# Kernel tuning notes

Measured on AMD Instinct MI355X. Metric: run time of the kernel, lower is better.

Reference implementation:

```python
import jax, jax.numpy as jnp
import numpy as np

NUM_SLOTS = 4096
NUM_CLUSTER = 10
SLOT_DIM = 64
EPS = 1e-8
N_ITER = 3
LN_EPS = 1e-5


def _ln(x, g, b):
    m = jnp.mean(x, axis=-1, keepdims=True)
    v = jnp.var(x, axis=-1, keepdims=True)
    return (x - m) / jnp.sqrt(v + LN_EPS) * g + b


def setup_inputs() -> dict:
    key = jax.random.key(0)
    ks = jax.random.split(key, 24)
    d, S = SLOT_DIM, NUM_SLOTS
    s = d ** -0.5
    f32 = jnp.float32
    return {
        "cluster_centers": jax.random.normal(ks[0], (NUM_CLUSTER, d), f32),
        "Wk": jax.random.normal(ks[1], (d, d), f32) * s,
        "bk": jnp.zeros((d,), f32),
        "Wq": jax.random.normal(ks[2], (d, d), f32) * s,
        "bq": jnp.zeros((d,), f32),
        "Wv": jax.random.normal(ks[3], (d, d), f32) * s,
        "bv": jnp.zeros((d,), f32),
        "cc_g": jnp.ones((d,), f32),
        "cc_b": jnp.zeros((d,), f32),
        "W_ih": jax.random.normal(ks[4], (3 * d, d), f32) * s,
        "W_hh": jax.random.normal(ks[5], (3 * d, d), f32) * s,
        "b_ih": jnp.zeros((3 * d,), f32),
        "b_hh": jnp.zeros((3 * d,), f32),
        "ln_g": jnp.ones((d,), f32),
        "ln_b": jnp.zeros((d,), f32),
        "W1": jax.random.normal(ks[6], (2 * d, d), f32) * s,
        "b1": jnp.zeros((2 * d,), f32),
        "W2": jax.random.normal(ks[7], (d, 2 * d), f32) * (2 * d) ** -0.5,
        "b2": jnp.zeros((d,), f32),
        "Wa": jax.random.normal(ks[8], (S, d, d), f32) * s,
        "ba": jnp.zeros((S, d), f32),
        "Wb": jax.random.normal(ks[9], (S, d, d), f32) * s,
        "bb": jnp.zeros((S, d), f32),
    }


def reference(cluster_centers, Wk, bk, Wq, bq, Wv, bv, cc_g, cc_b,
              W_ih, W_hh, b_ih, b_hh, ln_g, ln_b, W1, b1, W2, b2,
              Wa, ba, Wb, bb):
    temp = SLOT_DIM ** -0.5
    k = cluster_centers @ Wk.T + bk          # [N, d]
    v = cluster_centers @ Wv.T + bv          # [N, d]
    cc = cluster_centers
    for _ in range(N_ITER):
        cc_prev = cc
        q = _ln(cc, cc_g, cc_b) @ Wq.T + bq  # [N, d]
        attn = jnp.einsum('nd,md->nm', k, q) * temp
        attn = jax.nn.softmax(attn, axis=0) + EPS
        attn = attn / jnp.sum(attn, axis=-1, keepdims=True)
        updates = attn @ v                   # [N, d]
        # PyTorch GRUCell
        gi = updates @ W_ih.T + b_ih
        gh = cc_prev @ W_hh.T + b_hh
        ir, iz, inn = jnp.split(gi, 3, axis=-1)
        hr, hz, hn = jnp.split(gh, 3, axis=-1)
        r = jax.nn.sigmoid(ir + hr)
        z = jax.nn.sigmoid(iz + hz)
        n = jnp.tanh(inn + r * hn)
        cc = (1.0 - z) * n + z * cc_prev
        # residual MLP
        h = _ln(cc, ln_g, ln_b)
        cc = cc + jax.nn.relu(h @ W1.T + b1) @ W2.T + b2
    # per-slot 2-layer MLP + max over the 10 clusters, vectorized over slots
    h = jax.nn.relu(jnp.einsum('sij,nj->sni', Wa, cc) + ba[:, None, :])  # [S, N, d]
    out = jnp.einsum('sij,snj->sni', Wb, h) + bb[:, None, :]             # [S, N, d]
    return jnp.max(out, axis=1)                                          # [S, d]
```

## Files before the change

kernel.cpp:

```cpp
#include <hip/hip_runtime.h>
#include <math.h>

#define NCLU 10
#define D    64
#define NSLOT 4096

typedef unsigned int   u32;
typedef unsigned short u16;

typedef __attribute__((ext_vector_type(8))) short  bf16x8;
typedef __attribute__((ext_vector_type(4))) float  f32x4;

__device__ __forceinline__ u16 f2bf_rne(float f) {
    u32 u = __float_as_uint(f);
    return (u16)((u + 0x7fffu + ((u >> 16) & 1u)) >> 16);
}

__device__ __forceinline__ float dotb64(const float* __restrict__ xrow, const float4* w4) {
    const float4* x4 = (const float4*)xrow;
    float a0 = 0.f, a1 = 0.f, a2 = 0.f, a3 = 0.f;
#pragma unroll
    for (int jj = 0; jj < 16; ++jj) {
        float4 xv = x4[jj], wv = w4[jj];
        a0 += wv.x * xv.x; a1 += wv.y * xv.y; a2 += wv.z * xv.z; a3 += wv.w * xv.w;
    }
    return (a0 + a1) + (a2 + a3);
}
__device__ __forceinline__ float dotb128(const float* __restrict__ xrow, const float4* w4) {
    const float4* x4 = (const float4*)xrow;
    float a0 = 0.f, a1 = 0.f, a2 = 0.f, a3 = 0.f;
#pragma unroll
    for (int jj = 0; jj < 32; ++jj) {
        float4 xv = x4[jj], wv = w4[jj];
        a0 += wv.x * xv.x; a1 += wv.y * xv.y; a2 += wv.z * xv.z; a3 += wv.w * xv.w;
    }
    return (a0 + a1) + (a2 + a3);
}

__device__ __forceinline__ float wred(float v) {
#pragma unroll
    for (int off = 32; off > 0; off >>= 1) v += __shfl_xor(v, off);
    return v;
}

__global__ __launch_bounds__(640) void phase1_kernel(
    const float* __restrict__ cc0,
    const float* __restrict__ Wk, const float* __restrict__ bk,
    const float* __restrict__ Wq, const float* __restrict__ bq,
    const float* __restrict__ Wv, const float* __restrict__ bv,
    const float* __restrict__ cc_g, const float* __restrict__ cc_b,
    const float* __restrict__ W_ih, const float* __restrict__ W_hh,
    const float* __restrict__ b_ih, const float* __restrict__ b_hh,
    const float* __restrict__ ln_g, const float* __restrict__ ln_b,
    const float* __restrict__ W1, const float* __restrict__ b1,
    const float* __restrict__ W2, const float* __restrict__ b2,
    float* __restrict__ cc_out)
{
    const int t = threadIdx.x;
    const int w = t >> 6;
    const int i = t & 63;

    __shared__ float ccl[NCLU][64];
    __shared__ float xl[NCLU][64];
    __shared__ float kl[NCLU][64];
    __shared__ float vl[NCLU][64];
    __shared__ float ql[NCLU][68];
    __shared__ float al[NCLU][12];
    __shared__ float ul[NCLU][64];
    __shared__ float hl[NCLU][64];
    __shared__ float tl[NCLU][128];
    __shared__ float gl[6][NCLU][64];
    __shared__ float dl[NCLU][64];

    const float g_cc = cc_g[i], b_cc = cc_b[i];
    const float g_ln = ln_g[i], b_ln = ln_b[i];

    const float* srcp;
    float bias0 = 0.f, biask = 0.f;
    if (w == 0)      { srcp = Wq + i * 64;                     bias0 = bq[i]; }
    else if (w <= 3) { srcp = W_ih + ((w - 1) * 64 + i) * 64;  bias0 = b_ih[(w - 1) * 64 + i]; }
    else if (w <= 6) { srcp = W_hh + ((w - 4) * 64 + i) * 64;  bias0 = b_hh[(w - 4) * 64 + i]; }
    else if (w == 7) { srcp = Wk + i * 64;                     biask = bk[i]; }
    else if (w == 8) { srcp = Wv + i * 64;                     biask = bv[i]; }
    else             { srcp = W2 + i * 128;                    bias0 = b2[i]; }

    float4 w4[32];
#pragma unroll
    for (int jj = 0; jj < 16; ++jj) w4[jj] = ((const float4*)srcp)[jj];
#pragma unroll
    for (int jj = 16; jj < 32; ++jj) w4[jj] = make_float4(0.f, 0.f, 0.f, 0.f);
    if (w == 9) {
#pragma unroll
        for (int jj = 16; jj < 32; ++jj) w4[jj] = ((const float4*)srcp)[jj];
    }

    float c = cc0[w * 64 + i];
    ccl[w][i] = c;
    __syncthreads();

    if (w == 7) {
#pragma unroll
        for (int n = 0; n < NCLU; ++n) kl[n][i] = dotb64(&ccl[n][0], w4) + biask;
    } else if (w == 8) {
#pragma unroll
        for (int n = 0; n < NCLU; ++n) vl[n][i] = dotb64(&ccl[n][0], w4) + biask;
    }
    __syncthreads();

    if (w == 7) {
        const float4* p = (const float4*)(W1 + i * 64);
#pragma unroll
        for (int jj = 0; jj < 16; ++jj) w4[jj] = p[jj];
        bias0 = b1[i];
    } else if (w == 8) {
        const float4* p = (const float4*)(W1 + (64 + i) * 64);
#pragma unroll
        for (int jj = 0; jj < 16; ++jj) w4[jj] = p[jj];
        bias0 = b1[64 + i];
    }

    for (int it = 0; it < 3; ++it) {
        {
            float s1 = wred(c), s2 = wred(c * c);
            float mu = s1 * (1.f / 64.f);
            float va = s2 * (1.f / 64.f) - mu * mu;
            xl[w][i] = (c - mu) * rsqrtf(va + 1e-5f) * g_cc + b_cc;
        }
        __syncthreads();

        if (w == 0) {
#pragma unroll
            for (int n = 0; n < NCLU; ++n) ql[n][i] = dotb64(&xl[n][0], w4) + bias0;
        } else if (w >= 4 && w <= 6) {
#pragma unroll
            for (int n = 0; n < NCLU; ++n) gl[w - 1][n][i] = dotb64(&ccl[n][0], w4) + bias0;
        }
        __syncthreads();

        if (i < NCLU) {
            const float4* kf = (const float4*)&kl[w][0];
            const float4* qf = (const float4*)&ql[i][0];
            float a0 = 0.f, a1 = 0.f, a2 = 0.f, a3 = 0.f;
#pragma unroll
            for (int jj = 0; jj < 16; ++jj) {
                float4 kv = kf[jj], qv = qf[jj];
                a0 += kv.x * qv.x; a1 += kv.y * qv.y; a2 += kv.z * qv.z; a3 += kv.w * qv.w;
            }
            al[w][i] = ((a0 + a1) + (a2 + a3)) * 0.125f;
        }
        __syncthreads();

        if (t < NCLU) {
            float mx = -1e30f;
#pragma unroll
            for (int nn = 0; nn < NCLU; ++nn) mx = fmaxf(mx, al[nn][t]);
            float e[NCLU]; float s = 0.f;
#pragma unroll
            for (int nn = 0; nn < NCLU; ++nn) { e[nn] = __expf(al[nn][t] - mx); s += e[nn]; }
            float inv = 1.f / s;
#pragma unroll
            for (int nn = 0; nn < NCLU; ++nn) al[nn][t] = e[nn] * inv + 1e-8f;
        }
        __syncthreads();
        if (t < NCLU) {
            float s = 0.f;
#pragma unroll
            for (int m = 0; m < NCLU; ++m) s += al[t][m];
            float inv = 1.f / s;
#pragma unroll
            for (int m = 0; m < NCLU; ++m) al[t][m] *= inv;
        }
        __syncthreads();

        {
            float u = 0.f;
#pragma unroll
            for (int m = 0; m < NCLU; ++m) u += al[w][m] * vl[m][i];
            ul[w][i] = u;
        }
        __syncthreads();

        if (w >= 1 && w <= 3) {
#pragma unroll
            for (int n = 0; n < NCLU; ++n) gl[w - 1][n][i] = dotb64(&ul[n][0], w4) + bias0;
        }
        __syncthreads();

        {
            float ir = gl[0][w][i], iz = gl[1][w][i], inn = gl[2][w][i];
            float hr = gl[3][w][i], hz = gl[4][w][i], hn = gl[5][w][i];
            float r = 1.f / (1.f + __expf(-(ir + hr)));
            float z = 1.f / (1.f + __expf(-(iz + hz)));
            float nn2 = tanhf(inn + r * hn);
            c = (1.f - z) * nn2 + z * c;
        }

        {
            float s1 = wred(c), s2 = wred(c * c);
            float mu = s1 * (1.f / 64.f);
            float va = s2 * (1.f / 64.f) - mu * mu;
            hl[w][i] = (c - mu) * rsqrtf(va + 1e-5f) * g_ln + b_ln;
        }
        __syncthreads();

        if (w == 7) {
#pragma unroll
            for (int n = 0; n < NCLU; ++n) tl[n][i] = fmaxf(dotb64(&hl[n][0], w4) + bias0, 0.f);
        } else if (w == 8) {
#pragma unroll
            for (int n = 0; n < NCLU; ++n) tl[n][64 + i] = fmaxf(dotb64(&hl[n][0], w4) + bias0, 0.f);
        }
        __syncthreads();

        if (w == 9) {
#pragma unroll
            for (int n = 0; n < NCLU; ++n) dl[n][i] = dotb128(&tl[n][0], w4) + bias0;
        }
        __syncthreads();

        c += dl[w][i];
        ccl[w][i] = c;
        __syncthreads();
    }

    cc_out[w * 64 + i] = c;
}

#define WSTRIDE 72
__global__ __launch_bounds__(64) void phase2_kernel(
    const float* __restrict__ Wa, const float* __restrict__ ba,
    const float* __restrict__ Wb, const float* __restrict__ bb,
    const float* __restrict__ cc, float* __restrict__ out)
{
    const int s = blockIdx.x;
    const int l = threadIdx.x;
    const int quad = l >> 4;
    const int lc   = l & 15;

    __shared__ u16 Wlds[64 * WSTRIDE];
    __shared__ u16 hT[16 * WSTRIDE];

    const float* wa = Wa + (size_t)s * 4096;
    const float* wb = Wb + (size_t)s * 4096;

    float4 rg[16];
#pragma unroll
    for (int cch = 0; cch < 16; ++cch)
        rg[cch] = *(const float4*)(wa + cch * 256 + l * 4);

#pragma unroll
    for (int cch = 0; cch < 16; ++cch) {
        int row = cch * 4 + quad;
        u32 p0 = (u32)f2bf_rne(rg[cch].x) | ((u32)f2bf_rne(rg[cch].y) << 16);
        u32 p1 = (u32)f2bf_rne(rg[cch].z) | ((u32)f2bf_rne(rg[cch].w) << 16);
        uint2 pk; pk.x = p0; pk.y = p1;
        *(uint2*)(&Wlds[row * WSTRIDE + lc * 4]) = pk;
    }

#pragma unroll
    for (int cch = 0; cch < 16; ++cch)
        rg[cch] = *(const float4*)(wb + cch * 256 + l * 4);

    f32x4 acc[4];
#pragma unroll
    for (int mt = 0; mt < 4; ++mt) acc[mt] = (f32x4){0.f, 0.f, 0.f, 0.f};

#pragma unroll
    for (int kt = 0; kt < 2; ++kt) {
        bf16x8 bf;
        if (lc < NCLU) {
            const float* cp = cc + lc * 64 + kt * 32 + quad * 8;
            float4 c0 = *(const float4*)cp;
            float4 c1 = *(const float4*)(cp + 4);
            bf[0] = (short)f2bf_rne(c0.x); bf[1] = (short)f2bf_rne(c0.y);
            bf[2] = (short)f2bf_rne(c0.z); bf[3] = (short)f2bf_rne(c0.w);
            bf[4] = (short)f2bf_rne(c1.x); bf[5] = (short)f2bf_rne(c1.y);
            bf[6] = (short)f2bf_rne(c1.z); bf[7] = (short)f2bf_rne(c1.w);
        } else {
#pragma unroll
            for (int j = 0; j < 8; ++j) bf[j] = 0;
        }
#pragma unroll
        for (int mt = 0; mt < 4; ++mt) {
            bf16x8 af = *(const bf16x8*)(&Wlds[(16 * mt + lc) * WSTRIDE + kt * 32 + quad * 8]);
            acc[mt] = __builtin_amdgcn_mfma_f32_16x16x32_bf16(af, bf, acc[mt], 0, 0, 0);
        }
    }

#pragma unroll
    for (int mt = 0; mt < 4; ++mt) {
        float4 bav = *(const float4*)(ba + s * 64 + 16 * mt + quad * 4);
        u16 h0 = f2bf_rne(fmaxf(acc[mt][0] + bav.x, 0.f));
        u16 h1 = f2bf_rne(fmaxf(acc[mt][1] + bav.y, 0.f));
        u16 h2 = f2bf_rne(fmaxf(acc[mt][2] + bav.z, 0.f));
        u16 h3 = f2bf_rne(fmaxf(acc[mt][3] + bav.w, 0.f));
        uint2 pk; pk.x = (u32)h0 | ((u32)h1 << 16); pk.y = (u32)h2 | ((u32)h3 << 16);
        *(uint2*)(&hT[lc * WSTRIDE + 16 * mt + quad * 4]) = pk;
    }

#pragma unroll
    for (int cch = 0; cch < 16; ++cch) {
        int row = cch * 4 + quad;
        u32 p0 = (u32)f2bf_rne(rg[cch].x) | ((u32)f2bf_rne(rg[cch].y) << 16);
        u32 p1 = (u32)f2bf_rne(rg[cch].z) | ((u32)f2bf_rne(rg[cch].w) << 16);
        uint2 pk; pk.x = p0; pk.y = p1;
        *(uint2*)(&Wlds[row * WSTRIDE + lc * 4]) = pk;
    }

    f32x4 acc2[4];
#pragma unroll
    for (int mt = 0; mt < 4; ++mt) acc2[mt] = (f32x4){0.f, 0.f, 0.f, 0.f};
#pragma unroll
    for (int kt = 0; kt < 2; ++kt) {
        bf16x8 bf = *(const bf16x8*)(&hT[lc * WSTRIDE + kt * 32 + quad * 8]);
#pragma unroll
        for (int mt = 0; mt < 4; ++mt) {
            bf16x8 af = *(const bf16x8*)(&Wlds[(16 * mt + lc) * WSTRIDE + kt * 32 + quad * 8]);
            acc2[mt] = __builtin_amdgcn_mfma_f32_16x16x32_bf16(af, bf, acc2[mt], 0, 0, 0);
        }
    }

    const float NEG = -3.0e38f;
#pragma unroll
    for (int mt = 0; mt < 4; ++mt) {
#pragma unroll
        for (int r = 0; r < 4; ++r) {
            float v = (lc < NCLU) ? acc2[mt][r] : NEG;
#pragma unroll
            for (int off = 1; off < 16; off <<= 1)
                v = fmaxf(v, __shfl_xor(v, off));
            acc2[mt][r] = v;
        }
    }

    if (lc < 4) {
#pragma unroll
        for (int mt = 0; mt < 4; ++mt) {
            int row = 16 * mt + 4 * quad + lc;
            out[s * 64 + row] = acc2[mt][lc] + bb[s * 64 + row];
        }
    }
}

extern "C" void kernel_launch(void* const* d_in, const int* in_sizes, int n_in,
                              void* d_out, int out_size, void* d_ws, size_t ws_size,
                              hipStream_t stream) {
    const float* cc0  = (const float*)d_in[0];
    const float* Wk   = (const float*)d_in[1];
    const float* bk   = (const float*)d_in[2];
    const float* Wq   = (const float*)d_in[3];
    const float* bq   = (const float*)d_in[4];
    const float* Wv   = (const float*)d_in[5];
    const float* bv   = (const float*)d_in[6];
    const float* ccg  = (const float*)d_in[7];
    const float* ccb  = (const float*)d_in[8];
    const float* Wih  = (const float*)d_in[9];
    const float* Whh  = (const float*)d_in[10];
    const float* bih  = (const float*)d_in[11];
    const float* bhh  = (const float*)d_in[12];
    const float* lng  = (const float*)d_in[13];
    const float* lnb  = (const float*)d_in[14];
    const float* W1   = (const float*)d_in[15];
    const float* b1   = (const float*)d_in[16];
    const float* W2   = (const float*)d_in[17];
    const float* b2   = (const float*)d_in[18];
    const float* Wa   = (const float*)d_in[19];
    const float* ba   = (const float*)d_in[20];
    const float* Wb   = (const float*)d_in[21];
    const float* bb   = (const float*)d_in[22];

    float* cc_ws = (float*)d_ws;
    float* out   = (float*)d_out;

    hipLaunchKernelGGL(phase1_kernel, dim3(1), dim3(640), 0, stream,
                       cc0, Wk, bk, Wq, bq, Wv, bv, ccg, ccb,
                       Wih, Whh, bih, bhh, lng, lnb, W1, b1, W2, b2, cc_ws);

    hipLaunchKernelGGL(phase2_kernel, dim3(NSLOT), dim3(64), 0, stream,
                       Wa, ba, Wb, bb, cc_ws, out);
}
```

Measured before the change: 261.3 us.

## Use bf16 MFMA for phase1 small matmuls and split W2 across two waves

Replaces the per-thread fp32 dot products in the cluster-update kernel with bf16 MFMA 16x16x32 matmuls. Weight fragments are packed to bf16 in registers, and LDS rows are padded to a stride of 68. The 128-wide W2 reduction is split between waves 8 and 9, with the two partial outputs summed. This shortens the serial dependency chain and cuts register pressure (launch bounds now request 3 blocks), at the cost of bf16 precision on the iterative GRU/MLP updates.

```diff
diff --git a/kernel.cpp b/kernel.cpp
--- a/kernel.cpp
+++ b/kernel.cpp
@@ -16,25 +16,13 @@
     return (u16)((u + 0x7fffu + ((u >> 16) & 1u)) >> 16);
 }
 
-__device__ __forceinline__ float dotb64(const float* __restrict__ xrow, const float4* w4) {
-    const float4* x4 = (const float4*)xrow;
-    float a0 = 0.f, a1 = 0.f, a2 = 0.f, a3 = 0.f;
-#pragma unroll
-    for (int jj = 0; jj < 16; ++jj) {
-        float4 xv = x4[jj], wv = w4[jj];
-        a0 += wv.x * xv.x; a1 += wv.y * xv.y; a2 += wv.z * xv.z; a3 += wv.w * xv.w;
-    }
-    return (a0 + a1) + (a2 + a3);
-}
-__device__ __forceinline__ float dotb128(const float* __restrict__ xrow, const float4* w4) {
-    const float4* x4 = (const float4*)xrow;
-    float a0 = 0.f, a1 = 0.f, a2 = 0.f, a3 = 0.f;
-#pragma unroll
-    for (int jj = 0; jj < 32; ++jj) {
-        float4 xv = x4[jj], wv = w4[jj];
-        a0 += wv.x * xv.x; a1 += wv.y * xv.y; a2 += wv.z * xv.z; a3 += wv.w * xv.w;
-    }
-    return (a0 + a1) + (a2 + a3);
+__device__ __forceinline__ bf16x8 pack8(float4 a, float4 b) {
+    bf16x8 r;
+    r[0] = (short)f2bf_rne(a.x); r[1] = (short)f2bf_rne(a.y);
+    r[2] = (short)f2bf_rne(a.z); r[3] = (short)f2bf_rne(a.w);
+    r[4] = (short)f2bf_rne(b.x); r[5] = (short)f2bf_rne(b.y);
+    r[6] = (short)f2bf_rne(b.z); r[7] = (short)f2bf_rne(b.w);
+    return r;
 }
 
 __device__ __forceinline__ float wred(float v) {
@@ -43,7 +31,74 @@
     return v;
 }
 
-__global__ __launch_bounds__(640) void phase1_kernel(
+__device__ __forceinline__ void load_afrags64(bf16x8 a[4][2], const float* __restrict__ W,
+                                              int lc, int quad) {
+#pragma unroll
+    for (int mt = 0; mt < 4; ++mt)
+#pragma unroll
+        for (int kt = 0; kt < 2; ++kt) {
+            const float* p = W + (16 * mt + lc) * 64 + kt * 32 + quad * 8;
+            a[mt][kt] = pack8(*(const float4*)p, *(const float4*)(p + 4));
+        }
+}
+
+__device__ __forceinline__ void load_afrags128(bf16x8 a[4][2], const float* __restrict__ W,
+                                               int ktbase, int lc, int quad) {
+#pragma unroll
+    for (int mt = 0; mt < 4; ++mt)
+#pragma unroll
+        for (int kt = 0; kt < 2; ++kt) {
+            const float* p = W + (16 * mt + lc) * 128 + (ktbase + kt) * 32 + quad * 8;
+            a[mt][kt] = pack8(*(const float4*)p, *(const float4*)(p + 4));
+        }
+}
+
+__device__ __forceinline__ bf16x8 bfrag(const float* __restrict__ xbase, int xstride,
+                                        int lc, int quad, int ktglob) {
+    if (lc < NCLU) {
+        const float* p = xbase + lc * xstride + ktglob * 32 + quad * 8;
+        return pack8(*(const float4*)p, *(const float4*)(p + 4));
+    }
+    bf16x8 z;
+#pragma unroll
+    for (int j = 0; j < 8; ++j) z[j] = 0;
+    return z;
+}
+
+__device__ __forceinline__ void mm_apply(const bf16x8 a[4][2], const float* __restrict__ xbase,
+                                         int xstride, int ktbase,
+                                         float* __restrict__ obase, int ostride, int ooff,
+                                         const float* __restrict__ bias, bool do_relu,
+                                         int lc, int quad) {
+    f32x4 acc[4];
+#pragma unroll
+    for (int mt = 0; mt < 4; ++mt) acc[mt] = (f32x4){0.f, 0.f, 0.f, 0.f};
+#pragma unroll
+    for (int kt = 0; kt < 2; ++kt) {
+        bf16x8 b = bfrag(xbase, xstride, lc, quad, ktbase + kt);
+#pragma unroll
+        for (int mt = 0; mt < 4; ++mt)
+            acc[mt] = __builtin_amdgcn_mfma_f32_16x16x32_bf16(a[mt][kt], b, acc[mt], 0, 0, 0);
+    }
+    if (lc < NCLU) {
+#pragma unroll
+        for (int mt = 0; mt < 4; ++mt) {
+            float4 o;
+            o.x = acc[mt][0]; o.y = acc[mt][1]; o.z = acc[mt][2]; o.w = acc[mt][3];
+            if (bias) {
+                float4 bv = *(const float4*)(bias + 16 * mt + 4 * quad);
+                o.x += bv.x; o.y += bv.y; o.z += bv.z; o.w += bv.w;
+            }
+            if (do_relu) {
+                o.x = fmaxf(o.x, 0.f); o.y = fmaxf(o.y, 0.f);
+                o.z = fmaxf(o.z, 0.f); o.w = fmaxf(o.w, 0.f);
+            }
+            *(float4*)(obase + lc * ostride + ooff + 16 * mt + 4 * quad) = o;
+        }
+    }
+}
+
+__global__ __launch_bounds__(640, 3) void phase1_kernel(
     const float* __restrict__ cc0,
     const float* __restrict__ Wk, const float* __restrict__ bk,
     const float* __restrict__ Wq, const float* __restrict__ bq,
@@ -59,65 +114,53 @@
     const int t = threadIdx.x;
     const int w = t >> 6;
     const int i = t & 63;
-
-    __shared__ float ccl[NCLU][64];
-    __shared__ float xl[NCLU][64];
-    __shared__ float kl[NCLU][64];
-    __shared__ float vl[NCLU][64];
+    const int quad = i >> 4;
+    const int lc   = i & 15;
+
+    __shared__ float ccl[NCLU][68];
+    __shared__ float xl[NCLU][68];
+    __shared__ float kl[NCLU][68];
+    __shared__ float vl[NCLU][68];
     __shared__ float ql[NCLU][68];
+    __shared__ float ul[NCLU][68];
+    __shared__ float hl[NCLU][68];
+    __shared__ float dl9[NCLU][68];
+    __shared__ float dl8[NCLU][68];
+    __shared__ float tl[NCLU][132];
+    __shared__ float gl[6][NCLU][68];
     __shared__ float al[NCLU][12];
-    __shared__ float ul[NCLU][64];
-    __shared__ float hl[NCLU][64];
-    __shared__ float tl[NCLU][128];
-    __shared__ float gl[6][NCLU][64];
-    __shared__ float dl[NCLU][64];
 
     const float g_cc = cc_g[i], b_cc = cc_b[i];
     const float g_ln = ln_g[i], b_ln = ln_b[i];
 
-    const float* srcp;
-    float bias0 = 0.f, biask = 0.f;
-    if (w == 0)      { srcp = Wq + i * 64;                     bias0 = bq[i]; }
-    else if (w <= 3) { srcp = W_ih + ((w - 1) * 64 + i) * 64;  bias0 = b_ih[(w - 1) * 64 + i]; }
-    else if (w <= 6) { srcp = W_hh + ((w - 4) * 64 + i) * 64;  bias0 = b_hh[(w - 4) * 64 + i]; }
-    else if (w == 7) { srcp = Wk + i * 64;                     biask = bk[i]; }
-    else if (w == 8) { srcp = Wv + i * 64;                     biask = bv[i]; }
-    else             { srcp = W2 + i * 128;                    bias0 = b2[i]; }
-
-    float4 w4[32];
-#pragma unroll
-    for (int jj = 0; jj < 16; ++jj) w4[jj] = ((const float4*)srcp)[jj];
-#pragma unroll
-    for (int jj = 16; jj < 32; ++jj) w4[jj] = make_float4(0.f, 0.f, 0.f, 0.f);
-    if (w == 9) {
-#pragma unroll
-        for (int jj = 16; jj < 32; ++jj) w4[jj] = ((const float4*)srcp)[jj];
-    }
+    bf16x8 afrA[4][2], afrB[4][2];
+#pragma unroll
+    for (int mt = 0; mt < 4; ++mt)
+#pragma unroll
+        for (int kt = 0; kt < 2; ++kt) {
+#pragma unroll
+            for (int j = 0; j < 8; ++j) { afrA[mt][kt][j] = 0; afrB[mt][kt][j] = 0; }
+        }
+
+    const float* biasA = nullptr;
+    if (w == 0)      { load_afrags64(afrA, Wq, lc, quad);                    biasA = bq; }
+    else if (w <= 3) { load_afrags64(afrA, W_ih + (w - 1) * 64 * 64, lc, quad); biasA = b_ih + (w - 1) * 64; }
+    else if (w <= 6) { load_afrags64(afrA, W_hh + (w - 4) * 64 * 64, lc, quad); biasA = b_hh + (w - 4) * 64; }
+    else if (w == 7) { load_afrags64(afrA, Wk, lc, quad); }
+    else if (w == 8) { load_afrags64(afrA, Wv, lc, quad);
+                       load_afrags128(afrB, W2, 2, lc, quad); }
+    else             { load_afrags128(afrA, W2, 0, lc, quad); biasA = b2; }
 
     float c = cc0[w * 64 + i];
     ccl[w][i] = c;
     __syncthreads();
 
-    if (w == 7) {
-#pragma unroll
-        for (int n = 0; n < NCLU; ++n) kl[n][i] = dotb64(&ccl[n][0], w4) + biask;
-    } else if (w == 8) {
-#pragma unroll
-        for (int n = 0; n < NCLU; ++n) vl[n][i] = dotb64(&ccl[n][0], w4) + biask;
-    }
+    if (w == 7)      mm_apply(afrA, &ccl[0][0], 68, 0, &kl[0][0], 68, 0, bk, false, lc, quad);
+    else if (w == 8) mm_apply(afrA, &ccl[0][0], 68, 0, &vl[0][0], 68, 0, bv, false, lc, quad);
     __syncthreads();
 
-    if (w == 7) {
-        const float4* p = (const float4*)(W1 + i * 64);
-#pragma unroll
-        for (int jj = 0; jj < 16; ++jj) w4[jj] = p[jj];
-        bias0 = b1[i];
-    } else if (w == 8) {
-        const float4* p = (const float4*)(W1 + (64 + i) * 64);
-#pragma unroll
-        for (int jj = 0; jj < 16; ++jj) w4[jj] = p[jj];
-        bias0 = b1[64 + i];
-    }
+    if (w == 7)      { load_afrags64(afrA, W1, lc, quad);            biasA = b1; }
+    else if (w == 8) { load_afrags64(afrA, W1 + 64 * 64, lc, quad);  biasA = b1 + 64; }
 
     for (int it = 0; it < 3; ++it) {
         {
@@ -128,13 +171,10 @@
         }
         __syncthreads();
 
-        if (w == 0) {
-#pragma unroll
-            for (int n = 0; n < NCLU; ++n) ql[n][i] = dotb64(&xl[n][0], w4) + bias0;
-        } else if (w >= 4 && w <= 6) {
-#pragma unroll
-            for (int n = 0; n < NCLU; ++n) gl[w - 1][n][i] = dotb64(&ccl[n][0], w4) + bias0;
-        }
+        if (w == 0)
+            mm_apply(afrA, &xl[0][0], 68, 0, &ql[0][0], 68, 0, biasA, false, lc, quad);
+        else if (w >= 4 && w <= 6)
+            mm_apply(afrA, &ccl[0][0], 68, 0, &gl[w - 1][0][0], 68, 0, biasA, false, lc, quad);
         __syncthreads();
 
         if (i < NCLU) {
@@ -180,10 +220,8 @@
         }
         __syncthreads();
 
-        if (w >= 1 && w <= 3) {
-#pragma unroll
-            for (int n = 0; n < NCLU; ++n) gl[w - 1][n][i] = dotb64(&ul[n][0], w4) + bias0;
-        }
+        if (w >= 1 && w <= 3)
+            mm_apply(afrA, &ul[0][0], 68, 0, &gl[w - 1][0][0], 68, 0, biasA, false, lc, quad);
         __syncthreads();
 
         {
@@ -193,9 +231,7 @@
             float z = 1.f / (1.f + __expf(-(iz + hz)));
             float nn2 = tanhf(inn + r * hn);
             c = (1.f - z) * nn2 + z * c;
-        }
-
-        {
+
             float s1 = wred(c), s2 = wred(c * c);
             float mu = s1 * (1.f / 64.f);
             float va = s2 * (1.f / 64.f) - mu * mu;
@@ -203,22 +239,19 @@
         }
         __syncthreads();
 
-        if (w == 7) {
-#pragma unroll
-            for (int n = 0; n < NCLU; ++n) tl[n][i] = fmaxf(dotb64(&hl[n][0], w4) + bias0, 0.f);
-        } else if (w == 8) {
-#pragma unroll
-            for (int n = 0; n < NCLU; ++n) tl[n][64 + i] = fmaxf(dotb64(&hl[n][0], w4) + bias0, 0.f);
-        }
-        __syncthreads();
-
-        if (w == 9) {
-#pragma unroll
-            for (int n = 0; n < NCLU; ++n) dl[n][i] = dotb128(&tl[n][0], w4) + bias0;
-        }
-        __syncthreads();
-
-        c += dl[w][i];
+        if (w == 7)
+            mm_apply(afrA, &hl[0][0], 68, 0, &tl[0][0], 132, 0, biasA, true, lc, quad);
+        else if (w == 8)
+            mm_apply(afrA, &hl[0][0], 68, 0, &tl[0][0], 132, 64, biasA, true, lc, quad);
+        __syncthreads();
+
+        if (w == 9)
+            mm_apply(afrA, &tl[0][0], 132, 0, &dl9[0][0], 68, 0, biasA, false, lc, quad);
+        else if (w == 8)
+            mm_apply(afrB, &tl[0][0], 132, 2, &dl8[0][0], 68, 0, nullptr, false, lc, quad);
+        __syncthreads();
+
+        c += dl9[w][i] + dl8[w][i];
         ccl[w][i] = c;
         __syncthreads();
     }
@@ -270,12 +303,7 @@
         bf16x8 bf;
         if (lc < NCLU) {
             const float* cp = cc + lc * 64 + kt * 32 + quad * 8;
-            float4 c0 = *(const float4*)cp;
-            float4 c1 = *(const float4*)(cp + 4);
-            bf[0] = (short)f2bf_rne(c0.x); bf[1] = (short)f2bf_rne(c0.y);
-            bf[2] = (short)f2bf_rne(c0.z); bf[3] = (short)f2bf_rne(c0.w);
-            bf[4] = (short)f2bf_rne(c1.x); bf[5] = (short)f2bf_rne(c1.y);
-            bf[6] = (short)f2bf_rne(c1.z); bf[7] = (short)f2bf_rne(c1.w);
+            bf = pack8(*(const float4*)cp, *(const float4*)(cp + 4));
         } else {
 #pragma unroll
             for (int j = 0; j < 8; ++j) bf[j] = 0;
```

Measured after the change: 219.5 us. -16.0%, faster.
